# Optimization experiments

Measured on AMD Instinct MI355X. Metric: run time of the kernel, lower is better.

## Reference

```python
import jax, jax.numpy as jnp
import numpy as np

B, S, HID = 2, 2048, 2048
NH, HD, RD = 16, 128, 64
KVC, QC = 512, 1536


def _apply_rope(t):
    # t: [B, H, S, R]; standard half-split rotary embedding
    R = t.shape[-1]
    s = t.shape[-2]
    inv_freq = 1.0 / (10000.0 ** (jnp.arange(0, R, 2, dtype=jnp.float32) / R))  # [R/2]
    ang = jnp.arange(s, dtype=jnp.float32)[:, None] * inv_freq[None, :]  # [S, R/2]
    cos, sin = jnp.cos(ang), jnp.sin(ang)
    t1, t2 = t[..., : R // 2], t[..., R // 2 :]
    return jnp.concatenate([t1 * cos - t2 * sin, t2 * cos + t1 * sin], axis=-1)


def setup_inputs() -> dict:
    key = jax.random.key(0)
    ks = jax.random.split(key, 20)

    def lin(k, fan_in, fan_out):
        bound = 1.0 / np.sqrt(fan_in)
        kw, kb = jax.random.split(k)
        W = jax.random.uniform(kw, (fan_in, fan_out), jnp.float32, -bound, bound)
        b = jax.random.uniform(kb, (fan_out,), jnp.float32, -bound, bound)
        return W, b

    x = jax.random.normal(ks[0], (B, S, HID), jnp.float32)
    W_kvd, b_kvd = lin(ks[1], HID, KVC)
    W_ku, b_ku = lin(ks[2], KVC, NH * HD)
    W_vu, b_vu = lin(ks[3], KVC, NH * HD)
    W_kr, b_kr = lin(ks[4], KVC, NH * RD)
    W_qd, b_qd = lin(ks[5], HID, QC)
    W_qu, b_qu = lin(ks[6], QC, NH * HD)
    W_qr, b_qr = lin(ks[7], QC, NH * RD)
    W_o, b_o = lin(ks[8], NH * HD, HID)
    return dict(x=x, W_kvd=W_kvd, b_kvd=b_kvd, W_ku=W_ku, b_ku=b_ku,
                W_vu=W_vu, b_vu=b_vu, W_kr=W_kr, b_kr=b_kr,
                W_qd=W_qd, b_qd=b_qd, W_qu=W_qu, b_qu=b_qu,
                W_qr=W_qr, b_qr=b_qr, W_o=W_o, b_o=b_o)


def reference(x, W_kvd, b_kvd, W_ku, b_ku, W_vu, b_vu, W_kr, b_kr,
              W_qd, b_qd, W_qu, b_qu, W_qr, b_qr, W_o, b_o):
    b, s, _ = x.shape

    def heads(t, d):  # [B,S,NH*d] -> [B,NH,S,d]
        return t.reshape(b, s, NH, d).transpose(0, 2, 1, 3)

    kv_c = x @ W_kvd + b_kvd                     # [B,S,KVC]
    keys_c = heads(kv_c @ W_ku + b_ku, HD)       # [B,H,S,HD]
    values = heads(kv_c @ W_vu + b_vu, HD)
    keys_r = _apply_rope(heads(kv_c @ W_kr + b_kr, RD))

    q_c = x @ W_qd + b_qd                        # [B,S,QC]
    queries_c = heads(q_c @ W_qu + b_qu, HD)
    queries_r = _apply_rope(heads(q_c @ W_qr + b_qr, RD))

    q = jnp.concatenate([queries_c, queries_r], axis=-1)  # [B,H,S,HD+RD]
    k = jnp.concatenate([keys_c, keys_r], axis=-1)

    scale = 1.0 / np.sqrt(HD + RD)
    scores = jnp.einsum('bhqd,bhkd->bhqk', q, k) * scale
    causal = jnp.triu(jnp.ones((s, s), dtype=bool), k=1)
    scores = jnp.where(causal[None, None], jnp.float32(-1e9), scores)
    probs = jax.nn.softmax(scores, axis=-1)
    ctx = jnp.einsum('bhqk,bhkd->bhqd', probs, values)    # [B,H,S,HD]
    ctx = ctx.transpose(0, 2, 1, 3).reshape(b, s, NH * HD)
    return ctx @ W_o + b_o
```

## Files before the change

### kernel.cpp

```cpp
#include <hip/hip_runtime.h>
#include <math.h>

#define BB   2
#define SS   2048
#define HIDD 2048
#define NHH  16
#define HDD  128
#define RDD  64
#define KVCC 512
#define QCC  1536
#define DQK  192
#define MROWS 4096

using bf16x8 = __attribute__((ext_vector_type(8))) short;
using short4v = __attribute__((ext_vector_type(4))) short;
using f32x4  = __attribute__((ext_vector_type(4))) float;
using f32x16 = __attribute__((ext_vector_type(16))) float;

static __device__ __forceinline__ float b2f(short s) {
    unsigned u = ((unsigned)(unsigned short)s) << 16;
    union { unsigned u; float f; } v; v.u = u; return v.f;
}
static __device__ __forceinline__ short f2b(float f) {
    union { float f; unsigned u; } v; v.f = f;
    unsigned r = (v.u + 0x7fffu + ((v.u >> 16) & 1u)) >> 16;
    return (short)r;
}
static __device__ __forceinline__ unsigned cvtpk(float lo, float hi) {
    unsigned r;
    asm("v_cvt_pk_bf16_f32 %0, %1, %2" : "=v"(r) : "v"(lo), "v"(hi));
    return r;
}

#define GLOAD16(gsrc, ldst) \
    __builtin_amdgcn_global_load_lds((const __attribute__((address_space(1))) void*)(gsrc), \
                                     (__attribute__((address_space(3))) void*)(ldst), 16, 0, 0)

__global__ void cvt_kernel(const float* __restrict__ in, short* __restrict__ out) {
    int i = (blockIdx.x * blockDim.x + threadIdx.x) * 4;
    float4 v = *(const float4*)(in + i);
    short4v o;
    o[0] = f2b(v.x); o[1] = f2b(v.y); o[2] = f2b(v.z); o[3] = f2b(v.w);
    *(short4v*)(out + i) = o;
}

__global__ void wtrans_kernel(
    const float* __restrict__ W0, const float* __restrict__ W1,
    const float* __restrict__ W2, const float* __restrict__ W3,
    const float* __restrict__ W4, const float* __restrict__ W5,
    const float* __restrict__ W6, const float* __restrict__ W7,
    short* __restrict__ D0, short* __restrict__ D1,
    short* __restrict__ D2, short* __restrict__ D3) {
    __shared__ float t[32][33];
    int bid = blockIdx.x;
    const float* W; short* Dst; int K, N, lt;
    if (bid < 4096) {
        if (bid < 1024) { W = W0; Dst = D0;                        K = 2048; N = 512;  lt = bid; }
        else            { W = W1; Dst = D0 + (size_t)512 * 2048;   K = 2048; N = 1536; lt = bid - 1024; }
    } else if (bid < 6656) {
        if (bid < 5120)      { W = W2; Dst = D1;                       K = 512; N = 2048; lt = bid - 4096; }
        else if (bid < 6144) { W = W3; Dst = D1 + (size_t)2048 * 512;  K = 512; N = 2048; lt = bid - 5120; }
        else                 { W = W4; Dst = D1 + (size_t)4096 * 512;  K = 512; N = 1024; lt = bid - 6144; }
    } else if (bid < 11264) {
        if (bid < 9728) { W = W5; Dst = D2;                        K = 1536; N = 2048; lt = bid - 6656; }
        else            { W = W6; Dst = D2 + (size_t)2048 * 1536;  K = 1536; N = 1024; lt = bid - 9728; }
    } else { W = W7; Dst = D3; K = 2048; N = 2048; lt = bid - 11264; }
    int ntx = N >> 5;
    int n0 = (lt % ntx) * 32, k0 = (lt / ntx) * 32;
    int tx = threadIdx.x, ty = threadIdx.y;
#pragma unroll
    for (int i = 0; i < 4; i++)
        t[ty + i * 8][tx] = W[(size_t)(k0 + ty + i * 8) * N + n0 + tx];
    __syncthreads();
#pragma unroll
    for (int i = 0; i < 4; i++)
        Dst[(size_t)(n0 + ty + i * 8) * K + k0 + tx] = f2b(t[tx][ty + i * 8]);
}

template <int ID>
__global__ __launch_bounds__(256) void gemm128(
    const short* __restrict__ A, const short* __restrict__ Bt,
    const float* __restrict__ b0, const float* __restrict__ b1, const float* __restrict__ b2,
    void* __restrict__ C0, void* __restrict__ C1,
    int M, int N, int K) {
    __shared__ short Asm[4096];
    __shared__ short Bsm[4096];
    int tid = threadIdx.x, lane = tid & 63, w = tid >> 6;
    int wm = w >> 1, wn = w & 1;
    int m0 = blockIdx.y * 128, n0 = blockIdx.x * 128;
    int fr = lane & 15, fk = (lane >> 4) * 8;
    const short* Ag = A + (size_t)(m0 + (tid >> 2)) * K + (tid & 3) * 8;
    const short* Bg = Bt + (size_t)(n0 + (tid >> 2)) * K + (tid & 3) * 8;
    f32x4 acc[4][4] = {};
    for (int k0 = 0; k0 < K; k0 += 32) {
        __syncthreads();
        GLOAD16(Ag + k0, &Asm[tid * 8]);
        GLOAD16(Ag + k0 + (size_t)64 * K, &Asm[2048 + tid * 8]);
        GLOAD16(Bg + k0, &Bsm[tid * 8]);
        GLOAD16(Bg + k0 + (size_t)64 * K, &Bsm[2048 + tid * 8]);
        __syncthreads();
        bf16x8 af[4], bfv[4];
#pragma unroll
        for (int m = 0; m < 4; m++)
            af[m] = *(const bf16x8*)&Asm[(wm * 64 + m * 16 + fr) * 32 + fk];
#pragma unroll
        for (int n = 0; n < 4; n++)
            bfv[n] = *(const bf16x8*)&Bsm[(wn * 64 + n * 16 + fr) * 32 + fk];
#pragma unroll
        for (int m = 0; m < 4; m++)
#pragma unroll
            for (int n = 0; n < 4; n++)
                acc[m][n] = __builtin_amdgcn_mfma_f32_16x16x32_bf16(af[m], bfv[n], acc[m][n], 0, 0, 0);
    }
#pragma unroll
    for (int m = 0; m < 4; m++)
#pragma unroll
        for (int n = 0; n < 4; n++)
#pragma unroll
            for (int r = 0; r < 4; r++) {
                int row = m0 + wm * 64 + m * 16 + ((lane >> 4) << 2) + r;
                int col = n0 + wn * 64 + n * 16 + fr;
                float v = acc[m][n][r];
                if constexpr (ID == 0) {
                    ((float*)C0)[(size_t)row * N + col] = v + b0[col];
                } else if constexpr (ID == 1) {
                    if (col < KVCC)
                        ((short*)C0)[(size_t)row * KVCC + col] = f2b(v + b0[col]);
                    else
                        ((short*)C1)[(size_t)row * QCC + (col - KVCC)] = f2b(v + b1[col - KVCC]);
                } else if constexpr (ID == 2) {
                    int b = row >> 11, s = row & (SS - 1);
                    if (col < 2048) {
                        int h = col >> 7, d = col & 127;
                        ((short*)C0)[(((size_t)(b * NHH + h)) * SS + s) * DQK + d] = f2b(v + b0[col]);
                    } else if (col < 4096) {
                        int c = col - 2048; int h = c >> 7, d = c & 127;
                        ((short*)C1)[(((size_t)(b * NHH + h)) * HDD + d) * SS + s] = f2b(v + b1[c]);
                    } else {
                        int c = col - 4096; int h = c >> 6, d = c & 63;
                        ((short*)C0)[(((size_t)(b * NHH + h)) * SS + s) * DQK + HDD + d] = f2b(v + b2[c]);
                    }
                } else {
                    int b = row >> 11, s = row & (SS - 1);
                    if (col < 2048) {
                        int h = col >> 7, d = col & 127;
                        ((short*)C0)[(((size_t)(b * NHH + h)) * SS + s) * DQK + d] = f2b(v + b0[col]);
                    } else {
                        int c = col - 2048; int h = c >> 6, d = c & 63;
                        ((short*)C0)[(((size_t)(b * NHH + h)) * SS + s) * DQK + HDD + d] = f2b(v + b1[c]);
                    }
                }
            }
}

__global__ void rope_kernel(short* __restrict__ Tk, short* __restrict__ Tq) {
    int idx = blockIdx.x * blockDim.x + threadIdx.x;
    const int HALF = BB * NHH * SS * 32;
    short* T = (idx < HALF) ? Tk : Tq;
    int id = (idx < HALF) ? idx : idx - HALF;
    int i = id & 31;
    int s = (id >> 5) & (SS - 1);
    int bh = id >> 16;
    short* p = T + ((size_t)bh * SS + s) * DQK + HDD;
    float t1 = b2f(p[i]), t2 = b2f(p[i + 32]);
    float inv = exp2f(-(float)i * 0.41524101186092034f);
    float ang = (float)s * inv;
    float sn, cs;
    sincosf(ang, &sn, &cs);
    p[i] = f2b(t1 * cs - t2 * sn);
    p[i + 32] = f2b(t2 * cs + t1 * sn);
}

__global__ __launch_bounds__(256, 2) void attn_kernel(
    const short* __restrict__ Q, const short* __restrict__ Kg,
    const short* __restrict__ Vt, short* __restrict__ ctx) {
    __shared__ short Ksm[64 * 192];
    __shared__ short Vsm[128 * 64];
    int tid = threadIdx.x, lane = tid & 63, w = tid >> 6;
    int hf = lane >> 5, l31 = lane & 31;
    int bid = blockIdx.x;
    int half = bid >> 8, a = (bid & 255) >> 5;
    int qt = half ? a : 15 - a;
    int bh = bid & 31;
    int bb = bh >> 4, hd = bh & 15;
    int q0 = qt * 128;
    const short* Qp = Q + (size_t)bh * SS * DQK;
    const short* Kp = Kg + (size_t)bh * SS * DQK;
    const char*  Vp = (const char*)(Vt + (size_t)bh * HDD * SS);
    int wr0 = q0 + w * 32;
    int qrow = wr0 + l31;
    const float scale = 0.07216878364870323f;
    const float L2E = 1.44269504088896f;

    bf16x8 qf[12];
#pragma unroll
    for (int s = 0; s < 12; s++)
        qf[s] = *(const bf16x8*)(Qp + (size_t)qrow * DQK + s * 16 + hf * 8);

    f32x16 acc[4] = {};
    float mrow = -1e30f, lsum = 0.f;
    int nt = 2 * qt + 2;

    bf16x8 vreg[4];
    auto stageK = [&](int key0) {
#pragma unroll
        for (int pp = 0; pp < 6; pp++) {
            int flat = pp * 4096 + tid * 16;
            int row = flat / 384, bir = flat - row * 384;
            const char* src = (const char*)Kp + (size_t)(key0 + row) * 384 + (bir ^ ((row & 7) << 4));
            GLOAD16(src, (char*)Ksm + flat);
        }
    };
    auto loadV = [&](int key0) {
#pragma unroll
        for (int c = 0; c < 4; c++) {
            int flat = c * 4096 + tid * 16;
            int d = flat >> 7, bik = flat & 127;
            vreg[c] = *(const bf16x8*)(Vp + (size_t)d * (SS * 2) + (size_t)key0 * 2 + bik);
        }
    };
    auto writeV = [&]() {
#pragma unroll
        for (int c = 0; c < 4; c++) {
            int flat = c * 4096 + tid * 16;
            int d = flat >> 7, bik = flat & 127;
            *(bf16x8*)((char*)Vsm + d * 128 + (bik ^ ((d & 7) << 4))) = vreg[c];
        }
    };

    stageK(0); loadV(0); writeV();
    __syncthreads();

    for (int t0 = 0; t0 < nt; t0++) {
        int key0 = t0 * 64;
        bool active = (key0 <= wr0 + 31);
        f32x16 sv0, sv1;
        if (active) {
            f32x16 z = {};
            sv0 = z; sv1 = z;
            int xr = (l31 & 7) << 4;
            __builtin_amdgcn_s_setprio(1);
#pragma unroll
            for (int s = 0; s < 12; s++) {
                bf16x8 k0 = *(const bf16x8*)((const char*)Ksm + l31 * 384 + ((s * 32 + hf * 16) ^ xr));
                bf16x8 k1 = *(const bf16x8*)((const char*)Ksm + (32 + l31) * 384 + ((s * 32 + hf * 16) ^ xr));
                sv0 = __builtin_amdgcn_mfma_f32_32x32x16_bf16(k0, qf[s], sv0, 0, 0, 0);
                sv1 = __builtin_amdgcn_mfma_f32_32x32x16_bf16(k1, qf[s], sv1, 0, 0, 0);
            }
            __builtin_amdgcn_s_setprio(0);
        }
        __syncthreads();
        bool pre = (t0 + 1 < nt);
        if (pre) { stageK(key0 + 64); loadV(key0 + 64); }
        if (active) {
            bool domask = (key0 + 63 > wr0);
            float p[32];
            float pmax = -1e30f;
#pragma unroll
            for (int t = 0; t < 2; t++)
#pragma unroll
                for (int r = 0; r < 16; r++) {
                    float v = (t ? sv1[r] : sv0[r]) * scale;
                    int key = key0 + 32 * t + (r & 3) + 8 * (r >> 2) + 4 * hf;
                    if (domask && key > qrow) v = -1e30f;
                    p[t * 16 + r] = v;
                    pmax = fmaxf(pmax, v);
                }
            pmax = fmaxf(pmax, __shfl_xor(pmax, 32, 64));
            if (__any(pmax > mrow + 8.f)) {
                float mn = fmaxf(mrow, pmax);
                float al = exp2f((mrow - mn) * L2E);
                mrow = mn;
                lsum *= al;
                float arl[16];
#pragma unroll
                for (int r = 0; r < 16; r++)
                    arl[r] = __shfl(al, (r & 3) + 8 * (r >> 2) + 4 * hf, 64);
#pragma unroll
                for (int n = 0; n < 4; n++)
#pragma unroll
                    for (int r = 0; r < 16; r++)
                        acc[n][r] *= arl[r];
            }
#pragma unroll
            for (int i = 0; i < 32; i++) {
                p[i] = exp2f((p[i] - mrow) * L2E);
                lsum += p[i];
            }
#pragma unroll
            for (int g = 0; g < 4; g++) {
                int base = (g >> 1) * 16 + (g & 1) * 8;
                unsigned a01 = cvtpk(p[base + 0], p[base + 1]);
                unsigned a23 = cvtpk(p[base + 2], p[base + 3]);
                unsigned b01 = cvtpk(p[base + 4], p[base + 5]);
                unsigned b23 = cvtpk(p[base + 6], p[base + 7]);
                unsigned s0 = hf ? a01 : b01, s1 = hf ? a23 : b23;
                unsigned r0 = (unsigned)__shfl_xor((int)s0, 32, 64);
                unsigned r1 = (unsigned)__shfl_xor((int)s1, 32, 64);
                union { unsigned u[4]; bf16x8 v; } af;
                af.u[0] = hf ? r0 : a01;
                af.u[1] = hf ? r1 : a23;
                af.u[2] = hf ? b01 : r0;
                af.u[3] = hf ? b23 : r1;
                __builtin_amdgcn_s_setprio(1);
#pragma unroll
                for (int n = 0; n < 4; n++) {
                    int d = n * 32 + l31;
                    bf16x8 vf = *(const bf16x8*)((const char*)Vsm + d * 128 + ((g * 32 + hf * 16) ^ ((d & 7) << 4)));
                    acc[n] = __builtin_amdgcn_mfma_f32_32x32x16_bf16(af.v, vf, acc[n], 0, 0, 0);
                }
                __builtin_amdgcn_s_setprio(0);
            }
        }
        __syncthreads();
        if (pre) writeV();
    }
    lsum += __shfl_xor(lsum, 32, 64);
    float rc = 1.0f / lsum;
    float rcl[16];
#pragma unroll
    for (int r = 0; r < 16; r++)
        rcl[r] = __shfl(rc, (r & 3) + 8 * (r >> 2) + 4 * hf, 64);
#pragma unroll
    for (int n = 0; n < 4; n++)
#pragma unroll
        for (int r = 0; r < 16; r++) {
            int row = wr0 + (r & 3) + 8 * (r >> 2) + 4 * hf;
            int d = n * 32 + l31;
            ctx[((size_t)(bb * SS + row)) * (NHH * HDD) + hd * HDD + d] = f2b(acc[n][r] * rcl[r]);
        }
}

extern "C" void kernel_launch(void* const* d_in, const int* in_sizes, int n_in,
                              void* d_out, int out_size, void* d_ws, size_t ws_size,
                              hipStream_t stream) {
    const float* x     = (const float*)d_in[0];
    const float* W_kvd = (const float*)d_in[1];  const float* b_kvd = (const float*)d_in[2];
    const float* W_ku  = (const float*)d_in[3];  const float* b_ku  = (const float*)d_in[4];
    const float* W_vu  = (const float*)d_in[5];  const float* b_vu  = (const float*)d_in[6];
    const float* W_kr  = (const float*)d_in[7];  const float* b_kr  = (const float*)d_in[8];
    const float* W_qd  = (const float*)d_in[9];  const float* b_qd  = (const float*)d_in[10];
    const float* W_qu  = (const float*)d_in[11]; const float* b_qu  = (const float*)d_in[12];
    const float* W_qr  = (const float*)d_in[13]; const float* b_qr  = (const float*)d_in[14];
    const float* W_o   = (const float*)d_in[15]; const float* b_o   = (const float*)d_in[16];
    float* out = (float*)d_out;

    char* p = (char*)d_ws;
    auto alloc = [&](size_t elems) {
        short* r = (short*)p;
        p += ((elems * 2) + 255) & ~(size_t)255;
        return r;
    };
    short* xb   = alloc((size_t)MROWS * HIDD);
    short* kvc  = alloc((size_t)MROWS * KVCC);
    short* qc   = alloc((size_t)MROWS * QCC);
    short* kbuf = alloc((size_t)BB * NHH * SS * DQK);
    short* qbuf = alloc((size_t)BB * NHH * SS * DQK);
    short* vtb  = alloc((size_t)BB * NHH * HDD * SS);
    short* ctx  = alloc((size_t)MROWS * NHH * HDD);
    short* Wt1  = alloc((size_t)2048 * 2048);
    short* Wt2  = alloc((size_t)5120 * 512);
    short* Wt3  = alloc((size_t)3072 * 1536);
    short* Wt4  = alloc((size_t)2048 * 2048);

    cvt_kernel<<<dim3((MROWS * HIDD) / 1024), dim3(256), 0, stream>>>(x, xb);
    dim3 tb(32, 8);
    wtrans_kernel<<<dim3(15360), tb, 0, stream>>>(
        W_kvd, W_qd, W_ku, W_vu, W_kr, W_qu, W_qr, W_o, Wt1, Wt2, Wt3, Wt4);

    gemm128<1><<<dim3(2048 / 128, MROWS / 128), 256, 0, stream>>>(
        xb, Wt1, b_kvd, b_qd, nullptr, kvc, qc, MROWS, 2048, 2048);
    gemm128<2><<<dim3(5120 / 128, MROWS / 128), 256, 0, stream>>>(
        kvc, Wt2, b_ku, b_vu, b_kr, kbuf, vtb, MROWS, 5120, 512);
    gemm128<3><<<dim3(3072 / 128, MROWS / 128), 256, 0, stream>>>(
        qc, Wt3, b_qu, b_qr, nullptr, qbuf, nullptr, MROWS, 3072, 1536);

    rope_kernel<<<dim3((2 * BB * NHH * SS * 32) / 256), dim3(256), 0, stream>>>(kbuf, qbuf);

    attn_kernel<<<dim3(512), 256, 0, stream>>>(qbuf, kbuf, vtb, ctx);

    gemm128<0><<<dim3(HIDD / 128, MROWS / 128), 256, 0, stream>>>(
        ctx, Wt4, b_o, nullptr, nullptr, out, nullptr, MROWS, HIDD, NHH * HDD);
}
```

Baseline: 434.3 us.

## Double-buffer K/V tiles in LDS with direct global-to-LDS V loads

Doubles the K and V shared-memory tiles in the attention kernel. The next tile's K and V are now prefetched into the alternate buffer at the start of each iteration, and V is loaded global-to-LDS with a swizzled source address instead of going through registers. This removes one of the two barriers per key tile and the register staging of V, so loads can overlap the QK and PV MFMA work. The cost is doubled LDS use (about 80KB per block), which may restrict occupancy at two blocks per CU. The cross-half max shuffle is also moved inside the rescale branch.

```diff
diff --git a/kernel.cpp b/kernel.cpp
--- a/kernel.cpp
+++ b/kernel.cpp
@@ -174,8 +174,8 @@
 __global__ __launch_bounds__(256, 2) void attn_kernel(
     const short* __restrict__ Q, const short* __restrict__ Kg,
     const short* __restrict__ Vt, short* __restrict__ ctx) {
-    __shared__ short Ksm[64 * 192];
-    __shared__ short Vsm[128 * 64];
+    __shared__ short Ksm[2][64 * 192];
+    __shared__ short Vsm[2][128 * 64];
     int tid = threadIdx.x, lane = tid & 63, w = tid >> 6;
     int hf = lane >> 5, l31 = lane & 31;
     int bid = blockIdx.x;
@@ -201,58 +201,47 @@
     float mrow = -1e30f, lsum = 0.f;
     int nt = 2 * qt + 2;
 
-    bf16x8 vreg[4];
-    auto stageK = [&](int key0) {
+    auto stageK = [&](int key0, int b) {
 #pragma unroll
         for (int pp = 0; pp < 6; pp++) {
             int flat = pp * 4096 + tid * 16;
             int row = flat / 384, bir = flat - row * 384;
             const char* src = (const char*)Kp + (size_t)(key0 + row) * 384 + (bir ^ ((row & 7) << 4));
-            GLOAD16(src, (char*)Ksm + flat);
+            GLOAD16(src, (char*)Ksm[b] + flat);
         }
     };
-    auto loadV = [&](int key0) {
+    auto stageV = [&](int key0, int b) {
 #pragma unroll
         for (int c = 0; c < 4; c++) {
             int flat = c * 4096 + tid * 16;
             int d = flat >> 7, bik = flat & 127;
-            vreg[c] = *(const bf16x8*)(Vp + (size_t)d * (SS * 2) + (size_t)key0 * 2 + bik);
+            const char* src = Vp + (size_t)d * (SS * 2) + (size_t)key0 * 2 + (bik ^ ((d & 7) << 4));
+            GLOAD16(src, (char*)Vsm[b] + flat);
         }
     };
-    auto writeV = [&]() {
-#pragma unroll
-        for (int c = 0; c < 4; c++) {
-            int flat = c * 4096 + tid * 16;
-            int d = flat >> 7, bik = flat & 127;
-            *(bf16x8*)((char*)Vsm + d * 128 + (bik ^ ((d & 7) << 4))) = vreg[c];
-        }
-    };
-
-    stageK(0); loadV(0); writeV();
+
+    stageK(0, 0); stageV(0, 0);
     __syncthreads();
 
     for (int t0 = 0; t0 < nt; t0++) {
         int key0 = t0 * 64;
+        int cur = t0 & 1;
+        if (t0 + 1 < nt) { stageK(key0 + 64, cur ^ 1); stageV(key0 + 64, cur ^ 1); }
         bool active = (key0 <= wr0 + 31);
-        f32x16 sv0, sv1;
         if (active) {
             f32x16 z = {};
-            sv0 = z; sv1 = z;
+            f32x16 sv0 = z, sv1 = z;
             int xr = (l31 & 7) << 4;
+            const char* Kb = (const char*)Ksm[cur];
             __builtin_amdgcn_s_setprio(1);
 #pragma unroll
             for (int s = 0; s < 12; s++) {
-                bf16x8 k0 = *(const bf16x8*)((const char*)Ksm + l31 * 384 + ((s * 32 + hf * 16) ^ xr));
-                bf16x8 k1 = *(const bf16x8*)((const char*)Ksm + (32 + l31) * 384 + ((s * 32 + hf * 16) ^ xr));
+                bf16x8 k0 = *(const bf16x8*)(Kb + l31 * 384 + ((s * 32 + hf * 16) ^ xr));
+                bf16x8 k1 = *(const bf16x8*)(Kb + (32 + l31) * 384 + ((s * 32 + hf * 16) ^ xr));
                 sv0 = __builtin_amdgcn_mfma_f32_32x32x16_bf16(k0, qf[s], sv0, 0, 0, 0);
                 sv1 = __builtin_amdgcn_mfma_f32_32x32x16_bf16(k1, qf[s], sv1, 0, 0, 0);
             }
             __builtin_amdgcn_s_setprio(0);
-        }
-        __syncthreads();
-        bool pre = (t0 + 1 < nt);
-        if (pre) { stageK(key0 + 64); loadV(key0 + 64); }
-        if (active) {
             bool domask = (key0 + 63 > wr0);
             float p[32];
             float pmax = -1e30f;
@@ -266,9 +255,9 @@
                     p[t * 16 + r] = v;
                     pmax = fmaxf(pmax, v);
                 }
-            pmax = fmaxf(pmax, __shfl_xor(pmax, 32, 64));
             if (__any(pmax > mrow + 8.f)) {
-                float mn = fmaxf(mrow, pmax);
+                float pc = fmaxf(pmax, __shfl_xor(pmax, 32, 64));
+                float mn = fmaxf(mrow, pc);
                 float al = exp2f((mrow - mn) * L2E);
                 mrow = mn;
                 lsum *= al;
@@ -287,6 +276,7 @@
                 p[i] = exp2f((p[i] - mrow) * L2E);
                 lsum += p[i];
             }
+            const char* Vb = (const char*)Vsm[cur];
 #pragma unroll
             for (int g = 0; g < 4; g++) {
                 int base = (g >> 1) * 16 + (g & 1) * 8;
@@ -306,14 +296,13 @@
 #pragma unroll
                 for (int n = 0; n < 4; n++) {
                     int d = n * 32 + l31;
-                    bf16x8 vf = *(const bf16x8*)((const char*)Vsm + d * 128 + ((g * 32 + hf * 16) ^ ((d & 7) << 4)));
+                    bf16x8 vf = *(const bf16x8*)(Vb + d * 128 + ((g * 32 + hf * 16) ^ ((d & 7) << 4)));
                     acc[n] = __builtin_amdgcn_mfma_f32_32x32x16_bf16(af.v, vf, acc[n], 0, 0, 0);
                 }
                 __builtin_amdgcn_s_setprio(0);
             }
         }
         __syncthreads();
-        if (pre) writeV();
     }
     lsum += __shfl_xor(lsum, 32, 64);
     float rc = 1.0f / lsum;
```

After: 417.2 us. 1.04x faster.
